# Performance work log

Hardware: AMD Instinct MI355X
Metric: run time of the kernel (lower is better)

The kernel has to match this reference:

```python
import jax, jax.numpy as jnp
import numpy as np

INPUT_DIM = 128
NUM_CLASSES = 10
MAX_DEPTH = 8
HID = 16            # effective_transform_output_dim
TEMP = 1.0
EFF_IN = INPUT_DIM + 2          # root features + parent score + grandparent score
N_INTERNAL = 2 ** MAX_DEPTH - 1  # 255, level-order stacked
N_LEAVES = 2 ** MAX_DEPTH        # 256
BATCH = 32768


def setup_inputs() -> dict:
    key = jax.random.key(0)
    ks = jax.random.split(key, 6)
    x = jax.random.normal(ks[0], (BATCH, INPUT_DIM), jnp.float32)
    path_prob = jnp.ones((BATCH, 1), jnp.float32)
    W1 = jax.random.normal(ks[1], (N_INTERNAL, EFF_IN, HID), jnp.float32) * (1.0 / np.sqrt(EFF_IN))
    b1 = jax.random.normal(ks[2], (N_INTERNAL, HID), jnp.float32) * 0.01
    w2 = jax.random.normal(ks[3], (N_INTERNAL, HID), jnp.float32) * (1.0 / np.sqrt(HID))
    b2 = jax.random.normal(ks[4], (N_INTERNAL,), jnp.float32) * 0.01
    leaf_logits = jax.random.normal(ks[5], (N_LEAVES, NUM_CLASSES), jnp.float32)
    return {"x": x, "path_prob": path_prob, "W1": W1, "b1": b1,
            "w2": w2, "b2": b2, "leaf_logits": leaf_logits}


def reference(x, path_prob, W1, b1, w2, b2, leaf_logits):
    """Depth-batched soft binary tree: all 2^d nodes at depth d are processed
    as one batched GEMM instead of the original sequential recursion."""
    B = x.shape[0]
    pp = path_prob                              # [B, n_nodes_at_depth]
    parent = jnp.zeros((B, 1), x.dtype)         # parent decision scores (0 => unused at depth 0)
    grandp = jnp.zeros((B, 1), x.dtype)         # grandparent scores (0 => unused at depth 0,1)
    for d in range(MAX_DEPTH):
        lo, hi = 2 ** d - 1, 2 ** (d + 1) - 1   # level-order slice of this depth's nodes
        W1d = W1[lo:hi]                          # [N, EFF_IN, HID]
        # concat([x, parent, grandparent]) @ W1d without materializing the concat
        h = jnp.einsum('be,neh->bnh', x, W1d[:, :INPUT_DIM, :])
        h = h + parent[:, :, None] * W1d[None, :, INPUT_DIM, :]
        h = h + grandp[:, :, None] * W1d[None, :, INPUT_DIM + 1, :]
        t = jax.nn.relu(h + b1[lo:hi][None])                       # [B, N, HID]
        score = jnp.einsum('bnh,nh->bn', t, w2[lo:hi]) + b2[lo:hi][None]  # [B, N]
        p = jax.nn.sigmoid(score / TEMP)
        n = pp.shape[1]
        # children: left gets p, right gets 1-p; level-order interleave
        pp = jnp.stack([pp * p, pp * (1.0 - p)], axis=-1).reshape(B, 2 * n)
        grandp = jnp.repeat(parent, 2, axis=1)   # child's grandparent = node's parent
        parent = jnp.repeat(score, 2, axis=1)    # child's parent_out = this node's raw score
    # leaves: sum_n path_prob[:, n] * output_logits[n]
    return jnp.einsum('bn,nc->bc', pp, leaf_logits)
```

## Files before the change

### kernel.cpp

```cpp
#include <hip/hip_runtime.h>
#include <math.h>

namespace {

typedef __attribute__((ext_vector_type(8))) __fp16 f16x8;
typedef __attribute__((ext_vector_type(4))) float f32x4;

constexpr int IN_DIM = 128;
constexpr int EFF    = 130 * 16;
constexpr int NODES  = 255;
constexpr int TS     = 64;
constexpr int BLOCK  = 256;
constexpr int NC     = 10;

__global__ __launch_bounds__(256) void prep_w1(const float* __restrict__ W1,
                                               f16x8* __restrict__ wfrag) {
    __shared__ float xs[IN_DIM * 16];
    const int n = blockIdx.x, tid = threadIdx.x;
    const float4* src = (const float4*)(W1 + (size_t)n * EFF);
    ((float4*)xs)[tid]       = src[tid];
    ((float4*)xs)[tid + 256] = src[tid + 256];
    __syncthreads();
    const int l = tid & 63, t = tid >> 6;
    const int k0 = t * 32 + (l >> 4) * 8, hid = l & 15;
    f16x8 hv;
    #pragma unroll
    for (int j = 0; j < 8; ++j)
        hv[j] = (__fp16)xs[(k0 + j) * 16 + hid];
    wfrag[(n * 4 + t) * 64 + l] = hv;
}

__global__ __launch_bounds__(BLOCK) __attribute__((amdgpu_waves_per_eu(2, 2)))
void tree_mfma(
    const float* __restrict__ x, const float* __restrict__ path_prob,
    const float* __restrict__ W1, const float* __restrict__ b1,
    const float* __restrict__ w2, const float* __restrict__ b2,
    const float* __restrict__ leaf_logits,
    const f16x8* __restrict__ wfrag,
    float* __restrict__ out)
{
    __shared__ float pp[128][TS];
    __shared__ float scbuf[112][TS];

    const int tid  = threadIdx.x;
    const int wv   = tid >> 6, l = tid & 63;
    const int quad = l >> 4,   col = l & 15;
    const int s0   = blockIdx.x * TS;

    if (tid < TS) pp[0][tid] = path_prob[s0 + tid];

    f16x8 xh[4][4];
    #pragma unroll
    for (int t = 0; t < 4; ++t)
        #pragma unroll
        for (int mt = 0; mt < 4; ++mt) {
            const float* xp = x + (size_t)(s0 + mt * 16 + col) * IN_DIM + t * 32 + quad * 8;
            float4 v0 = ((const float4*)xp)[0];
            float4 v1 = ((const float4*)xp)[1];
            float vv[8] = {v0.x, v0.y, v0.z, v0.w, v1.x, v1.y, v1.z, v1.w};
            f16x8 hv;
            #pragma unroll
            for (int j = 0; j < 8; ++j) hv[j] = (__fp16)vv[j];
            xh[t][mt] = hv;
        }

    const int wbase[3] = {0, 64, 80};

    const int first_n = (wv == 0) ? 0 : (wv == 1) ? 2 : (wv == 2) ? 5 : 6;
    f16x8 wh0 = wfrag[(size_t)first_n * 256 + l];

    for (int d = 0; d < 7; ++d) {
        const int nd = 1 << d;
        float (*scW)[TS]  = (float(*)[TS])&scbuf[wbase[d % 3]][0];
        float (*scP)[TS]  = (float(*)[TS])&scbuf[wbase[(d + 2) % 3]][0];
        float (*scP2)[TS] = (float(*)[TS])&scbuf[wbase[(d + 1) % 3]][0];
        const int stride = 128 >> d, half = 64 >> d;

        for (int nl = wv; nl < nd; nl += 4) {
            const int n = nd - 1 + nl;
            const int nn = (nl + 4 < nd) ? (n + 4) : (2 * nd - 1 + wv);

            const float4 b1q = ((const float4*)(b1 + n * 16))[quad];
            const float4 w2q = ((const float4*)(w2 + n * 16))[quad];
            const float4 wpq = ((const float4*)(W1 + (size_t)n * EFF + 128 * 16))[quad];
            const float4 wgq = ((const float4*)(W1 + (size_t)n * EFF + 129 * 16))[quad];
            const float  b2v = b2[n];
            const int    slot = nl * stride;
            const float  ppar = pp[slot][l];
            float par[4], gp[4];
            #pragma unroll
            for (int mt = 0; mt < 4; ++mt) {
                const int scol = mt * 16 + col;
                par[mt] = (d >= 1) ? scP[nl >> 1][scol] : 0.0f;
                gp[mt]  = (d >= 2) ? scP2[nl >> 2][scol] : 0.0f;
            }

            const f16x8* whp = wfrag + (size_t)n * 256 + l;
            f16x8 whc = wh0;

            f32x4 binit = {b1q.x, b1q.y, b1q.z, b1q.w};
            f32x4 acc[4] = {binit, binit, binit, binit};
            #pragma unroll
            for (int t = 0; t < 4; ++t) {
                f16x8 whn;
                if (t < 3) whn = whp[(t + 1) * 64];
                if (t == 2)
                    wh0 = wfrag[(size_t)nn * 256 + l];
                #pragma unroll
                for (int mt = 0; mt < 4; ++mt)
                    acc[mt] = __builtin_amdgcn_mfma_f32_16x16x32_f16(whc, xh[t][mt], acc[mt], 0, 0, 0);
                if (t < 3) whc = whn;
            }

            float score01[4];
            #pragma unroll
            for (int mt = 0; mt < 4; ++mt) {
                const f32x4 a = acc[mt];
                const float pa = par[mt], ga = gp[mt];
                float ts = 0.0f;
                #pragma unroll
                for (int r = 0; r < 4; ++r) {
                    const float wpr = (r == 0) ? wpq.x : (r == 1) ? wpq.y : (r == 2) ? wpq.z : wpq.w;
                    const float wgr = (r == 0) ? wgq.x : (r == 1) ? wgq.y : (r == 2) ? wgq.z : wgq.w;
                    const float w2r = (r == 0) ? w2q.x : (r == 1) ? w2q.y : (r == 2) ? w2q.z : w2q.w;
                    const float h = fmaf(pa, wpr, fmaf(ga, wgr, a[r]));
                    ts = fmaf(fmaxf(h, 0.0f), w2r, ts);
                }
                ts += __shfl_xor(ts, 16);
                ts += __shfl_xor(ts, 32);
                score01[mt] = ts;
            }
            const float sa = (quad & 1) ? score01[1] : score01[0];
            const float sb = (quad & 1) ? score01[3] : score01[2];
            const float sv = ((quad & 2) ? sb : sa) + b2v;

            scW[nl][l] = sv;
            const float p = 1.0f / (1.0f + __expf(-sv));
            pp[slot][l]        = ppar * p;
            pp[slot + half][l] = ppar * (1.0f - p);
        }
        __syncthreads();
    }

    float oacc[NC];
    #pragma unroll
    for (int c = 0; c < NC; ++c) oacc[c] = 0.0f;
    {
        float (*scP)[TS]  = (float(*)[TS])&scbuf[wbase[0]][0];
        float (*scP2)[TS] = (float(*)[TS])&scbuf[wbase[2]][0];

        for (int nl = wv; nl < 128; nl += 4) {
            const int n = 127 + nl;
            const int nn = (nl + 4 < 128) ? (n + 4) : 254;

            const float4 b1q = ((const float4*)(b1 + n * 16))[quad];
            const float4 w2q = ((const float4*)(w2 + n * 16))[quad];
            const float4 wpq = ((const float4*)(W1 + (size_t)n * EFF + 128 * 16))[quad];
            const float4 wgq = ((const float4*)(W1 + (size_t)n * EFF + 129 * 16))[quad];
            const float  b2v = b2[n];
            const float  ppar = pp[nl][l];
            float par[4], gp[4];
            #pragma unroll
            for (int mt = 0; mt < 4; ++mt) {
                const int scol = mt * 16 + col;
                par[mt] = scP[nl >> 1][scol];
                gp[mt]  = scP2[nl >> 2][scol];
            }

            const f16x8* whp = wfrag + (size_t)n * 256 + l;
            f16x8 whc = wh0;

            f32x4 binit = {b1q.x, b1q.y, b1q.z, b1q.w};
            f32x4 acc[4] = {binit, binit, binit, binit};
            #pragma unroll
            for (int t = 0; t < 4; ++t) {
                f16x8 whn;
                if (t < 3) whn = whp[(t + 1) * 64];
                if (t == 2)
                    wh0 = wfrag[(size_t)nn * 256 + l];
                #pragma unroll
                for (int mt = 0; mt < 4; ++mt)
                    acc[mt] = __builtin_amdgcn_mfma_f32_16x16x32_f16(whc, xh[t][mt], acc[mt], 0, 0, 0);
                if (t < 3) whc = whn;
            }

            float score01[4];
            #pragma unroll
            for (int mt = 0; mt < 4; ++mt) {
                const f32x4 a = acc[mt];
                const float pa = par[mt], ga = gp[mt];
                float ts = 0.0f;
                #pragma unroll
                for (int r = 0; r < 4; ++r) {
                    const float wpr = (r == 0) ? wpq.x : (r == 1) ? wpq.y : (r == 2) ? wpq.z : wpq.w;
                    const float wgr = (r == 0) ? wgq.x : (r == 1) ? wgq.y : (r == 2) ? wgq.z : wgq.w;
                    const float w2r = (r == 0) ? w2q.x : (r == 1) ? w2q.y : (r == 2) ? w2q.z : w2q.w;
                    const float h = fmaf(pa, wpr, fmaf(ga, wgr, a[r]));
                    ts = fmaf(fmaxf(h, 0.0f), w2r, ts);
                }
                ts += __shfl_xor(ts, 16);
                ts += __shfl_xor(ts, 32);
                score01[mt] = ts;
            }
            const float sa = (quad & 1) ? score01[1] : score01[0];
            const float sb = (quad & 1) ? score01[3] : score01[2];
            const float sv = ((quad & 2) ? sb : sa) + b2v;

            const float p = 1.0f / (1.0f + __expf(-sv));
            const float pL = ppar * p;
            const float pR = ppar * (1.0f - p);
            const float* llp = leaf_logits + (size_t)(2 * nl) * NC;
            #pragma unroll
            for (int c = 0; c < NC; ++c)
                oacc[c] = fmaf(pL, llp[c], fmaf(pR, llp[NC + c], oacc[c]));
        }
    }

    __syncthreads();
    {
        float* red = &scbuf[0][0];
        #pragma unroll
        for (int c = 0; c < NC; ++c)
            red[(wv * 64 + l) * NC + c] = oacc[c];
    }
    __syncthreads();
    {
        const float* red = &scbuf[0][0];
        for (int i = tid; i < TS * NC; i += BLOCK) {
            float v = red[i] + red[640 + i] + red[1280 + i] + red[1920 + i];
            out[(size_t)s0 * NC + i] = v;
        }
    }
}

}

extern "C" void kernel_launch(void* const* d_in, const int* in_sizes, int n_in,
                              void* d_out, int out_size, void* d_ws, size_t ws_size,
                              hipStream_t stream) {
    const float* x           = (const float*)d_in[0];
    const float* path_prob   = (const float*)d_in[1];
    const float* W1          = (const float*)d_in[2];
    const float* b1          = (const float*)d_in[3];
    const float* w2          = (const float*)d_in[4];
    const float* b2          = (const float*)d_in[5];
    const float* leaf_logits = (const float*)d_in[6];
    float* out = (float*)d_out;

    const int batch = in_sizes[0] / IN_DIM;
    f16x8* wfrag = (f16x8*)d_ws;

    hipLaunchKernelGGL(prep_w1, dim3(NODES), dim3(256), 0, stream, W1, wfrag);
    hipLaunchKernelGGL(tree_mfma, dim3(batch / TS), dim3(BLOCK), 0, stream,
                       x, path_prob, W1, b1, w2, b2, leaf_logits, wfrag, out);
}
```

Baseline: 151.4 us.

## Halve sample tile to 32 and prefetch full next-node weight fragments

Shrinks each block's sample tile from 64 to 32 rows, which halves the per-wave x fragments and accumulators and raises the waves-per-EU target from 2 to 4. Each wave now loads all four weight fragments of its next node up front instead of streaming them one step at a time. Only half the lanes do useful writes, and weight-fragment traffic per sample doubles because twice as many blocks each reload every node's weights. The intent is to use higher occupancy to hide the latency of the serial per-node chain.

```diff
diff --git a/kernel.cpp b/kernel.cpp
--- a/kernel.cpp
+++ b/kernel.cpp
@@ -9,7 +9,7 @@
 constexpr int IN_DIM = 128;
 constexpr int EFF    = 130 * 16;
 constexpr int NODES  = 255;
-constexpr int TS     = 64;
+constexpr int TS     = 32;
 constexpr int BLOCK  = 256;
 constexpr int NC     = 10;
 
@@ -30,7 +30,7 @@
     wfrag[(n * 4 + t) * 64 + l] = hv;
 }
 
-__global__ __launch_bounds__(BLOCK) __attribute__((amdgpu_waves_per_eu(2, 2)))
+__global__ __launch_bounds__(BLOCK) __attribute__((amdgpu_waves_per_eu(4, 4)))
 void tree_mfma(
     const float* __restrict__ x, const float* __restrict__ path_prob,
     const float* __restrict__ W1, const float* __restrict__ b1,
@@ -45,15 +45,16 @@
     const int tid  = threadIdx.x;
     const int wv   = tid >> 6, l = tid & 63;
     const int quad = l >> 4,   col = l & 15;
+    const int lo32 = l & 31;
     const int s0   = blockIdx.x * TS;
 
     if (tid < TS) pp[0][tid] = path_prob[s0 + tid];
 
-    f16x8 xh[4][4];
+    f16x8 xh[4][2];
     #pragma unroll
     for (int t = 0; t < 4; ++t)
         #pragma unroll
-        for (int mt = 0; mt < 4; ++mt) {
+        for (int mt = 0; mt < 2; ++mt) {
             const float* xp = x + (size_t)(s0 + mt * 16 + col) * IN_DIM + t * 32 + quad * 8;
             float4 v0 = ((const float4*)xp)[0];
             float4 v1 = ((const float4*)xp)[1];
@@ -67,7 +68,9 @@
     const int wbase[3] = {0, 64, 80};
 
     const int first_n = (wv == 0) ? 0 : (wv == 1) ? 2 : (wv == 2) ? 5 : 6;
-    f16x8 wh0 = wfrag[(size_t)first_n * 256 + l];
+    f16x8 wcur[4];
+    #pragma unroll
+    for (int t = 0; t < 4; ++t) wcur[t] = wfrag[(size_t)first_n * 256 + t * 64 + l];
 
     for (int d = 0; d < 7; ++d) {
         const int nd = 1 << d;
@@ -80,41 +83,39 @@
             const int n = nd - 1 + nl;
             const int nn = (nl + 4 < nd) ? (n + 4) : (2 * nd - 1 + wv);
 
+            f16x8 wnext[4];
+            {
+                const f16x8* wnp = wfrag + (size_t)nn * 256 + l;
+                #pragma unroll
+                for (int t = 0; t < 4; ++t) wnext[t] = wnp[t * 64];
+            }
+
             const float4 b1q = ((const float4*)(b1 + n * 16))[quad];
             const float4 w2q = ((const float4*)(w2 + n * 16))[quad];
             const float4 wpq = ((const float4*)(W1 + (size_t)n * EFF + 128 * 16))[quad];
             const float4 wgq = ((const float4*)(W1 + (size_t)n * EFF + 129 * 16))[quad];
             const float  b2v = b2[n];
             const int    slot = nl * stride;
-            const float  ppar = pp[slot][l];
-            float par[4], gp[4];
-            #pragma unroll
-            for (int mt = 0; mt < 4; ++mt) {
+            const float  ppar = pp[slot][lo32];
+            float par[2], gp[2];
+            #pragma unroll
+            for (int mt = 0; mt < 2; ++mt) {
                 const int scol = mt * 16 + col;
                 par[mt] = (d >= 1) ? scP[nl >> 1][scol] : 0.0f;
                 gp[mt]  = (d >= 2) ? scP2[nl >> 2][scol] : 0.0f;
             }
 
-            const f16x8* whp = wfrag + (size_t)n * 256 + l;
-            f16x8 whc = wh0;
-
             f32x4 binit = {b1q.x, b1q.y, b1q.z, b1q.w};
-            f32x4 acc[4] = {binit, binit, binit, binit};
+            f32x4 acc[2] = {binit, binit};
             #pragma unroll
             for (int t = 0; t < 4; ++t) {
-                f16x8 whn;
-                if (t < 3) whn = whp[(t + 1) * 64];
-                if (t == 2)
-                    wh0 = wfrag[(size_t)nn * 256 + l];
-                #pragma unroll
-                for (int mt = 0; mt < 4; ++mt)
-                    acc[mt] = __builtin_amdgcn_mfma_f32_16x16x32_f16(whc, xh[t][mt], acc[mt], 0, 0, 0);
-                if (t < 3) whc = whn;
-            }
-
-            float score01[4];
-            #pragma unroll
-            for (int mt = 0; mt < 4; ++mt) {
+                acc[0] = __builtin_amdgcn_mfma_f32_16x16x32_f16(wcur[t], xh[t][0], acc[0], 0, 0, 0);
+                acc[1] = __builtin_amdgcn_mfma_f32_16x16x32_f16(wcur[t], xh[t][1], acc[1], 0, 0, 0);
+            }
+
+            float score01[2];
+            #pragma unroll
+            for (int mt = 0; mt < 2; ++mt) {
                 const f32x4 a = acc[mt];
                 const float pa = par[mt], ga = gp[mt];
                 float ts = 0.0f;
@@ -130,14 +131,17 @@
                 ts += __shfl_xor(ts, 32);
                 score01[mt] = ts;
             }
-            const float sa = (quad & 1) ? score01[1] : score01[0];
-            const float sb = (quad & 1) ? score01[3] : score01[2];
-            const float sv = ((quad & 2) ? sb : sa) + b2v;
-
-            scW[nl][l] = sv;
-            const float p = 1.0f / (1.0f + __expf(-sv));
-            pp[slot][l]        = ppar * p;
-            pp[slot + half][l] = ppar * (1.0f - p);
+            const float sv = ((l & 16) ? score01[1] : score01[0]) + b2v;
+
+            if (l < 32) {
+                scW[nl][lo32] = sv;
+                const float p = 1.0f / (1.0f + __expf(-sv));
+                pp[slot][lo32]        = ppar * p;
+                pp[slot + half][lo32] = ppar * (1.0f - p);
+            }
+
+            #pragma unroll
+            for (int t = 0; t < 4; ++t) wcur[t] = wnext[t];
         }
         __syncthreads();
     }
@@ -152,41 +156,39 @@
         for (int nl = wv; nl < 128; nl += 4) {
             const int n = 127 + nl;
             const int nn = (nl + 4 < 128) ? (n + 4) : 254;
+
+            f16x8 wnext[4];
+            {
+                const f16x8* wnp = wfrag + (size_t)nn * 256 + l;
+                #pragma unroll
+                for (int t = 0; t < 4; ++t) wnext[t] = wnp[t * 64];
+            }
 
             const float4 b1q = ((const float4*)(b1 + n * 16))[quad];
             const float4 w2q = ((const float4*)(w2 + n * 16))[quad];
             const float4 wpq = ((const float4*)(W1 + (size_t)n * EFF + 128 * 16))[quad];
             const float4 wgq = ((const float4*)(W1 + (size_t)n * EFF + 129 * 16))[quad];
             const float  b2v = b2[n];
-            const float  ppar = pp[nl][l];
-            float par[4], gp[4];
-            #pragma unroll
-            for (int mt = 0; mt < 4; ++mt) {
+            const float  ppar = pp[nl][lo32];
+            float par[2], gp[2];
+            #pragma unroll
+            for (int mt = 0; mt < 2; ++mt) {
                 const int scol = mt * 16 + col;
                 par[mt] = scP[nl >> 1][scol];
                 gp[mt]  = scP2[nl >> 2][scol];
             }
 
-            const f16x8* whp = wfrag + (size_t)n * 256 + l;
-            f16x8 whc = wh0;
-
             f32x4 binit = {b1q.x, b1q.y, b1q.z, b1q.w};
-            f32x4 acc[4] = {binit, binit, binit, binit};
+            f32x4 acc[2] = {binit, binit};
             #pragma unroll
             for (int t = 0; t < 4; ++t) {
-                f16x8 whn;
-                if (t < 3) whn = whp[(t + 1) * 64];
-                if (t == 2)
-                    wh0 = wfrag[(size_t)nn * 256 + l];
-                #pragma unroll
-                for (int mt = 0; mt < 4; ++mt)
-                    acc[mt] = __builtin_amdgcn_mfma_f32_16x16x32_f16(whc, xh[t][mt], acc[mt], 0, 0, 0);
-                if (t < 3) whc = whn;
-            }
-
-            float score01[4];
-            #pragma unroll
-            for (int mt = 0; mt < 4; ++mt) {
+                acc[0] = __builtin_amdgcn_mfma_f32_16x16x32_f16(wcur[t], xh[t][0], acc[0], 0, 0, 0);
+                acc[1] = __builtin_amdgcn_mfma_f32_16x16x32_f16(wcur[t], xh[t][1], acc[1], 0, 0, 0);
+            }
+
+            float score01[2];
+            #pragma unroll
+            for (int mt = 0; mt < 2; ++mt) {
                 const f32x4 a = acc[mt];
                 const float pa = par[mt], ga = gp[mt];
                 float ts = 0.0f;
@@ -202,9 +204,7 @@
                 ts += __shfl_xor(ts, 32);
                 score01[mt] = ts;
             }
-            const float sa = (quad & 1) ? score01[1] : score01[0];
-            const float sb = (quad & 1) ? score01[3] : score01[2];
-            const float sv = ((quad & 2) ? sb : sa) + b2v;
+            const float sv = ((l & 16) ? score01[1] : score01[0]) + b2v;
 
             const float p = 1.0f / (1.0f + __expf(-sv));
             const float pL = ppar * p;
@@ -213,21 +213,26 @@
             #pragma unroll
             for (int c = 0; c < NC; ++c)
                 oacc[c] = fmaf(pL, llp[c], fmaf(pR, llp[NC + c], oacc[c]));
+
+            #pragma unroll
+            for (int t = 0; t < 4; ++t) wcur[t] = wnext[t];
         }
     }
 
     __syncthreads();
     {
         float* red = &scbuf[0][0];
-        #pragma unroll
-        for (int c = 0; c < NC; ++c)
-            red[(wv * 64 + l) * NC + c] = oacc[c];
+        if (l < 32) {
+            #pragma unroll
+            for (int c = 0; c < NC; ++c)
+                red[(wv * 32 + lo32) * NC + c] = oacc[c];
+        }
     }
     __syncthreads();
     {
         const float* red = &scbuf[0][0];
         for (int i = tid; i < TS * NC; i += BLOCK) {
-            float v = red[i] + red[640 + i] + red[1280 + i] + red[1920 + i];
+            float v = red[i] + red[320 + i] + red[640 + i] + red[960 + i];
             out[(size_t)s0 * NC + i] = v;
         }
     }
```

After: 172.1 us. 1.14x slower.
